# Kernel tuning notes

Measured on AMD Instinct MI355X. Metric: run time of the kernel, lower is better.

Reference implementation:

```python
import jax, jax.numpy as jnp
import numpy as np

N = 4096
Q_DIM = K_DIM = V_DIM = OUT_DIM = ATTN_DIM = 512
NUM_HEADS = 8
HEAD_DIM = ATTN_DIM // NUM_HEADS
SCALE = float(HEAD_DIM) ** (-0.5)


def setup_inputs() -> dict:
    key = jax.random.key(0)
    ks = jax.random.split(key, 12)
    def lin(kw, kb, out_d, in_d):
        bound = 1.0 / np.sqrt(in_d)
        w = jax.random.uniform(kw, (out_d, in_d), jnp.float32, -bound, bound)
        b = jax.random.uniform(kb, (out_d,), jnp.float32, -bound, bound)
        return w, b
    wq_w, wq_b = lin(ks[0], ks[1], ATTN_DIM, Q_DIM)
    wk_w, wk_b = lin(ks[2], ks[3], ATTN_DIM, K_DIM)
    wv_w, wv_b = lin(ks[4], ks[5], ATTN_DIM, V_DIM)
    wo_w, wo_b = lin(ks[6], ks[7], OUT_DIM, ATTN_DIM)
    q = jax.random.normal(ks[8], (N, Q_DIM), jnp.float32)
    k = jax.random.normal(ks[9], (N, K_DIM), jnp.float32)
    v = jax.random.normal(ks[10], (N, V_DIM), jnp.float32)
    mask = jax.random.uniform(ks[11], (N, N)) < 0.1  # True = masked out
    return {"q": q, "k": k, "v": v, "mask": mask,
            "wq_w": wq_w, "wq_b": wq_b, "wk_w": wk_w, "wk_b": wk_b,
            "wv_w": wv_w, "wv_b": wv_b, "wo_w": wo_w, "wo_b": wo_b}


def reference(q, k, v, mask, wq_w, wq_b, wk_w, wk_b, wv_w, wv_b, wo_w, wo_b):
    # Linear projections (torch Linear: x @ W.T + b)
    qp = q @ wq_w.T + wq_b  # (N, A)
    kp = k @ wk_w.T + wk_b
    vp = v @ wv_w.T + wv_b
    # (N, A) -> (H, N, dh)
    qh = qp.reshape(N, NUM_HEADS, HEAD_DIM).transpose(1, 0, 2)
    kh = kp.reshape(N, NUM_HEADS, HEAD_DIM).transpose(1, 0, 2)
    vh = vp.reshape(N, NUM_HEADS, HEAD_DIM).transpose(1, 0, 2)
    attn = jnp.einsum('hnd,hmd->hnm', qh, kh) * SCALE  # (H, N, N)
    attn = jnp.where(mask[None, :, :], jnp.float32(-1e6), attn)
    attn = jax.nn.softmax(attn, axis=-1)
    o = jnp.einsum('hnm,hmd->hnd', attn, vh)  # (H, N, dh)
    o = o.transpose(1, 0, 2).reshape(N, ATTN_DIM)
    return o @ wo_w.T + wo_b  # (N, out_dim)
```

## Files before the change

kernel.cpp:

```cpp
#include <hip/hip_runtime.h>


typedef __attribute__((ext_vector_type(8))) short bf16x8;
typedef __attribute__((ext_vector_type(4))) float f32x4;

#define N_TOK 4096
#define QSCALE 0.18033688f

__device__ __forceinline__ unsigned short f2bf(float f) {
  unsigned u = __float_as_uint(f);
  return (unsigned short)((u + 0x7FFFu + ((u >> 16) & 1u)) >> 16);
}
__device__ __forceinline__ unsigned pack_bf16(float a, float b) {
  unsigned ua = __float_as_uint(a), ub = __float_as_uint(b);
  ua += 0x7FFFu + ((ua >> 16) & 1u);
  ub += 0x7FFFu + ((ub >> 16) & 1u);
  return (ua >> 16) | (ub & 0xFFFF0000u);
}
__device__ __forceinline__ f32x4 mfma16(bf16x8 a, bf16x8 b, f32x4 c) {
  return __builtin_amdgcn_mfma_f32_16x16x32_bf16(a, b, c, 0, 0, 0);
}
__device__ __forceinline__ float fast_exp2(float x) {
#if __has_builtin(__builtin_amdgcn_exp2f)
  return __builtin_amdgcn_exp2f(x);
#else
  return exp2f(x);
#endif
}

__global__ __launch_bounds__(256) void detect_kernel(
    const unsigned* __restrict__ mask, unsigned* __restrict__ flags) {
  __shared__ int s_bad;
  int t = threadIdx.x;
  if (t == 0) s_bad = 0;
  __syncthreads();
  if (mask[t] > 1u) atomicOr(&s_bad, 1);
  __syncthreads();
  if (t == 0) {
    flags[0] = 0;
    flags[1] = s_bad ? 1u : 0u;
  }
}

__global__ __launch_bounds__(256) void pack_mask_kernel(
    const void* __restrict__ m, unsigned long long* __restrict__ bits,
    const unsigned* __restrict__ flags) {
  int gt = blockIdx.x * 256 + threadIdx.x;
  int wave = gt >> 6;
  int lane = threadIdx.x & 63;
  int base = wave * 256;
  unsigned long long b0, b1, b2, b3;
  if (flags[1]) {
    const unsigned char* m8 = (const unsigned char*)m;
    b0 = __ballot(m8[base + 0 * 64 + lane] != 0);
    b1 = __ballot(m8[base + 1 * 64 + lane] != 0);
    b2 = __ballot(m8[base + 2 * 64 + lane] != 0);
    b3 = __ballot(m8[base + 3 * 64 + lane] != 0);
  } else {
    const int* m4 = (const int*)m;
    b0 = __ballot(m4[base + 0 * 64 + lane] != 0);
    b1 = __ballot(m4[base + 1 * 64 + lane] != 0);
    b2 = __ballot(m4[base + 2 * 64 + lane] != 0);
    b3 = __ballot(m4[base + 3 * 64 + lane] != 0);
  }
  if (lane < 4) {
    unsigned long long bl = lane == 0 ? b0 : lane == 1 ? b1 : lane == 2 ? b2 : b3;
    bits[wave * 4 + lane] = bl;
  }
}

template <int F32>
__device__ __forceinline__ void load16(const void* base, int idx,
                                       unsigned short* dst) {
  if (F32) {
    const float* p = (const float*)base + idx;
    float4 f0 = *(const float4*)(p + 0);
    float4 f1 = *(const float4*)(p + 4);
    float4 f2 = *(const float4*)(p + 8);
    float4 f3 = *(const float4*)(p + 12);
    unsigned* d = (unsigned*)dst;
    d[0] = pack_bf16(f0.x, f0.y); d[1] = pack_bf16(f0.z, f0.w);
    d[2] = pack_bf16(f1.x, f1.y); d[3] = pack_bf16(f1.z, f1.w);
    d[4] = pack_bf16(f2.x, f2.y); d[5] = pack_bf16(f2.z, f2.w);
    d[6] = pack_bf16(f3.x, f3.y); d[7] = pack_bf16(f3.z, f3.w);
  } else {
    const unsigned short* p = (const unsigned short*)base + idx;
    *(uint4*)dst = *(const uint4*)p;
    *(uint4*)(dst + 8) = *(const uint4*)(p + 8);
  }
}

template <int A32, int O32, int TRANS>
__device__ __forceinline__ void gemm_body(
    const void* __restrict__ A, const float* __restrict__ W,
    const float* __restrict__ bias, void* __restrict__ out, float oscale) {
  __shared__ unsigned short As[128 * 72];
  __shared__ unsigned short Bs[128 * 72];
  const int t = threadIdx.x;
  const int lane = t & 63, w = t >> 6;
  const int wm = w & 1, wn = w >> 1;
  const int q4 = lane >> 4, i15 = lane & 15;
  const int m0 = blockIdx.y * 128, n0 = blockIdx.x * 128;
  f32x4 acc[4][4] = {};
  const int sr = t >> 2;
  const int sc = (t & 3) * 16;
  for (int k0 = 0; k0 < 512; k0 += 64) {
    __syncthreads();
#pragma unroll
    for (int p = 0; p < 2; ++p) {
      int row = sr + p * 64;
      unsigned short ta[16], tb[16];
      load16<A32>(A, (m0 + row) * 512 + k0 + sc, ta);
      load16<1>(W, (n0 + row) * 512 + k0 + sc, tb);
      *(uint4*)(As + row * 72 + sc) = *(uint4*)ta;
      *(uint4*)(As + row * 72 + sc + 8) = *(uint4*)(ta + 8);
      *(uint4*)(Bs + row * 72 + sc) = *(uint4*)tb;
      *(uint4*)(Bs + row * 72 + sc + 8) = *(uint4*)(tb + 8);
    }
    __syncthreads();
#pragma unroll
    for (int ks = 0; ks < 2; ++ks) {
      bf16x8 af[4], bfr[4];
#pragma unroll
      for (int mt = 0; mt < 4; ++mt)
        af[mt] = *(const bf16x8*)(As + (wm * 64 + mt * 16 + i15) * 72 + q4 * 8 + ks * 32);
#pragma unroll
      for (int nt = 0; nt < 4; ++nt)
        bfr[nt] = *(const bf16x8*)(Bs + (wn * 64 + nt * 16 + i15) * 72 + q4 * 8 + ks * 32);
#pragma unroll
      for (int mt = 0; mt < 4; ++mt)
#pragma unroll
        for (int nt = 0; nt < 4; ++nt)
          acc[mt][nt] = mfma16(af[mt], bfr[nt], acc[mt][nt]);
    }
  }
#pragma unroll
  for (int nt = 0; nt < 4; ++nt) {
    int col = n0 + wn * 64 + nt * 16 + i15;
    float bv = bias[col];
    if (TRANS) {
      unsigned short* ob_ = (unsigned short*)out +
                            (size_t)(col >> 6) * (64 * N_TOK) +
                            (size_t)(col & 63) * N_TOK;
#pragma unroll
      for (int mt = 0; mt < 4; ++mt) {
        int rowb = m0 + wm * 64 + mt * 16 + q4 * 4;
        uint2 pr;
        pr.x = pack_bf16(acc[mt][nt][0] + bv, acc[mt][nt][1] + bv);
        pr.y = pack_bf16(acc[mt][nt][2] + bv, acc[mt][nt][3] + bv);
        *(uint2*)(ob_ + rowb) = pr;
      }
    } else {
#pragma unroll
      for (int mt = 0; mt < 4; ++mt) {
        int rowb = m0 + wm * 64 + mt * 16 + q4 * 4;
#pragma unroll
        for (int rr = 0; rr < 4; ++rr) {
          int idx = (rowb + rr) * 512 + col;
          float val = (acc[mt][nt][rr] + bv) * oscale;
          if (O32) ((float*)out)[idx] = val;
          else ((unsigned short*)out)[idx] = f2bf(val);
        }
      }
    }
  }
}

__global__ __launch_bounds__(256) void qkv_gemm_kernel(
    const float* __restrict__ q, const float* __restrict__ k,
    const float* __restrict__ v, const float* __restrict__ wq,
    const float* __restrict__ wk, const float* __restrict__ wv,
    const float* __restrict__ bq, const float* __restrict__ bk,
    const float* __restrict__ bv, unsigned short* __restrict__ outbase) {
  int z = blockIdx.z;
  if (z == 0) {
    gemm_body<1, 0, 0>(q, wq, bq, outbase, QSCALE);
  } else if (z == 1) {
    gemm_body<1, 0, 0>(k, wk, bk, outbase + (size_t)N_TOK * 512, 1.0f);
  } else {
    gemm_body<1, 0, 1>(v, wv, bv, outbase + 2ull * N_TOK * 512, 1.0f);
  }
}

__global__ __launch_bounds__(256) void out_gemm_kernel(
    const unsigned short* __restrict__ A, const float* __restrict__ W,
    const float* __restrict__ B, float* __restrict__ out) {
  gemm_body<0, 1, 0>(A, W, B, out, 1.0f);
}

__global__ __launch_bounds__(256, 2) void attn_kernel(
    const unsigned short* __restrict__ qp, const unsigned short* __restrict__ kp,
    const unsigned short* __restrict__ vpT,
    const unsigned long long* __restrict__ mbits,
    float* __restrict__ Op, float* __restrict__ dp) {
  __shared__ unsigned short Ks[2][64 * 64];
  __shared__ unsigned short Vt[2][64 * 64];
  const int t = threadIdx.x;
  const int l = t & 63, w = t >> 6;
  const int q4 = l >> 4, i15 = l & 15;
  const int iblk = blockIdx.x * 256;
  const int head = blockIdx.y;
  const int chunk = blockIdx.z;
  const int ch = head * 64;
  const int i0 = iblk + w * 64;
  const int ji = l >> 3;
  const int sg = l & 7;
  const int r0 = w * 2;
  const int j0base = chunk * 1024;
  bf16x8 qf[4][2];
#pragma unroll
  for (int nt = 0; nt < 4; ++nt) {
    const unsigned short* qr = qp + (size_t)(i0 + nt * 16 + i15) * 512 + ch;
#pragma unroll
    for (int ks = 0; ks < 2; ++ks)
      qf[nt][ks] = *(const bf16x8*)(qr + ks * 32 + q4 * 8);
  }
  const unsigned long long* mrow[4];
#pragma unroll
  for (int nt = 0; nt < 4; ++nt)
    mrow[nt] = mbits + (size_t)(i0 + nt * 16 + i15) * 64;
  f32x4 oacc[4][4] = {};
  float den[4] = {0.f, 0.f, 0.f, 0.f};
  const unsigned short* vbase = vpT + (size_t)head * (64 * N_TOK);
  uint4 kst[2], vst[2];
#pragma unroll
  for (int rr = 0; rr < 2; ++rr) {
    int row = (r0 + rr) * 8 + ji;
    kst[rr] = *(const uint4*)(kp + (size_t)(j0base + row) * 512 + ch + sg * 8);
    vst[rr] = *(const uint4*)(vbase + (size_t)row * N_TOK + j0base + sg * 8);
  }
  for (int jt = 0; jt < 16; ++jt) {
    unsigned short* KsB = Ks[jt & 1];
    unsigned short* VtB = Vt[jt & 1];
#pragma unroll
    for (int rr = 0; rr < 2; ++rr) {
      int r = r0 + rr;
      int row = r * 8 + ji;
      *(uint4*)(KsB + row * 64 + ((sg ^ ji ^ r) * 8)) = kst[rr];
      const unsigned* vs = (const unsigned*)&vst[rr];
#pragma unroll
      for (int c2 = 0; c2 < 2; ++c2) {
        int kg = (sg >> 2) * 4 + (sg & 1) * 2 + c2;
        int hh = (sg >> 1) & 1;
        *(uint2*)(VtB + row * 64 + ((kg ^ ji ^ r) * 8) + hh * 4) =
            make_uint2(vs[c2 * 2], vs[c2 * 2 + 1]);
      }
    }
    __syncthreads();
    {
      int jn = j0base + ((jt + 1) & 15) * 64;
#pragma unroll
      for (int rr = 0; rr < 2; ++rr) {
        int row = (r0 + rr) * 8 + ji;
        kst[rr] = *(const uint4*)(kp + (size_t)(jn + row) * 512 + ch + sg * 8);
        vst[rr] = *(const uint4*)(vbase + (size_t)row * N_TOK + jn + sg * 8);
      }
    }
    unsigned long long mw[4];
    int widx = chunk * 16 + jt;
#pragma unroll
    for (int nt = 0; nt < 4; ++nt) mw[nt] = mrow[nt][widx];
    bf16x8 Kf[4][2];
#pragma unroll
    for (int mtj = 0; mtj < 4; ++mtj) {
      int js = mtj * 16 + i15;
#pragma unroll
      for (int ksd = 0; ksd < 2; ++ksd) {
        int g = ksd * 4 + q4;
        Kf[mtj][ksd] =
            *(const bf16x8*)(KsB + js * 64 + ((g ^ (js & 7) ^ (js >> 3)) * 8));
      }
    }
    unsigned pk[4][8];
#pragma unroll
    for (int nt = 0; nt < 4; ++nt) {
      float dsum = 0.f;
#pragma unroll
      for (int mtj = 0; mtj < 4; ++mtj) {
        f32x4 s = {0.f, 0.f, 0.f, 0.f};
        s = mfma16(Kf[mtj][0], qf[nt][0], s);
        s = mfma16(Kf[mtj][1], qf[nt][1], s);
        unsigned nib = (unsigned)(mw[nt] >> (mtj * 16 + q4 * 4)) & 15u;
        float p0 = fast_exp2((nib & 1u) ? -200.f : s[0]);
        float p1 = fast_exp2((nib & 2u) ? -200.f : s[1]);
        float p2 = fast_exp2((nib & 4u) ? -200.f : s[2]);
        float p3 = fast_exp2((nib & 8u) ? -200.f : s[3]);
        dsum += (p0 + p1) + (p2 + p3);
        pk[nt][mtj * 2] = pack_bf16(p0, p1);
        pk[nt][mtj * 2 + 1] = pack_bf16(p2, p3);
      }
      den[nt] += dsum;
    }
    bf16x8 Vf[2][4];
#pragma unroll
    for (int ks = 0; ks < 2; ++ks)
#pragma unroll
      for (int mtd = 0; mtd < 4; ++mtd) {
        int d = mtd * 16 + i15;
        int kg = ks * 4 + q4;
        Vf[ks][mtd] =
            *(const bf16x8*)(VtB + d * 64 + ((kg ^ (d & 7) ^ (d >> 3)) * 8));
      }
#pragma unroll
    for (int nt = 0; nt < 4; ++nt) {
      union { unsigned u[4]; bf16x8 v; } pf0, pf1;
      pf0.u[0] = pk[nt][0]; pf0.u[1] = pk[nt][1];
      pf0.u[2] = pk[nt][2]; pf0.u[3] = pk[nt][3];
      pf1.u[0] = pk[nt][4]; pf1.u[1] = pk[nt][5];
      pf1.u[2] = pk[nt][6]; pf1.u[3] = pk[nt][7];
#pragma unroll
      for (int mtd = 0; mtd < 4; ++mtd) {
        oacc[mtd][nt] = mfma16(Vf[0][mtd], pf0.v, oacc[mtd][nt]);
        oacc[mtd][nt] = mfma16(Vf[1][mtd], pf1.v, oacc[mtd][nt]);
      }
    }
  }
  float* Opc = Op + ((size_t)(chunk * 8 + head) * N_TOK) * 64;
#pragma unroll
  for (int nt = 0; nt < 4; ++nt) {
    float dn = den[nt];
    dn += __shfl_xor(dn, 16);
    dn += __shfl_xor(dn, 32);
    int row = i0 + nt * 16 + i15;
#pragma unroll
    for (int mtd = 0; mtd < 4; ++mtd)
      *(f32x4*)(Opc + (size_t)row * 64 + mtd * 16 + q4 * 4) = oacc[mtd][nt];
    if (q4 == 0) dp[(size_t)(chunk * 8 + head) * N_TOK + row] = dn;
  }
}

__global__ __launch_bounds__(256) void reduce_kernel(
    const float* __restrict__ Op, const float* __restrict__ dp,
    unsigned short* __restrict__ ob) {
  int x = blockIdx.x * 256 + threadIdx.x;
  int i = x >> 7;
  int c = (x & 127) * 4;
  int h = c >> 6;
  int d = c & 63;
  const size_t CH = (size_t)8 * N_TOK * 64;
  size_t base = ((size_t)h * N_TOK + i) * 64 + d;
  float4 a0 = *(const float4*)(Op + base);
  float4 a1 = *(const float4*)(Op + CH + base);
  float4 a2 = *(const float4*)(Op + 2 * CH + base);
  float4 a3 = *(const float4*)(Op + 3 * CH + base);
  float den = dp[(size_t)h * N_TOK + i] + dp[(size_t)(8 + h) * N_TOK + i] +
              dp[(size_t)(16 + h) * N_TOK + i] + dp[(size_t)(24 + h) * N_TOK + i];
  float inv = 1.0f / den;
  float sx = (a0.x + a1.x + a2.x + a3.x) * inv;
  float sy = (a0.y + a1.y + a2.y + a3.y) * inv;
  float sz = (a0.z + a1.z + a2.z + a3.z) * inv;
  float sw = (a0.w + a1.w + a2.w + a3.w) * inv;
  uint2 o;
  o.x = pack_bf16(sx, sy);
  o.y = pack_bf16(sz, sw);
  *(uint2*)(ob + (size_t)i * 512 + c) = o;
}

extern "C" void kernel_launch(void* const* d_in, const int* in_sizes, int n_in,
                              void* d_out, int out_size, void* d_ws, size_t ws_size,
                              hipStream_t stream) {
  const float* q = (const float*)d_in[0];
  const float* k = (const float*)d_in[1];
  const float* v = (const float*)d_in[2];
  const void* mask = d_in[3];
  const float* wq = (const float*)d_in[4];
  const float* bq = (const float*)d_in[5];
  const float* wk = (const float*)d_in[6];
  const float* bk = (const float*)d_in[7];
  const float* wv = (const float*)d_in[8];
  const float* bv = (const float*)d_in[9];
  const float* wo = (const float*)d_in[10];
  const float* bo = (const float*)d_in[11];

  char* ws = (char*)d_ws;
  unsigned* flags = (unsigned*)ws;
  unsigned long long* mb = (unsigned long long*)(ws + 4096);
  unsigned short* qkvp = (unsigned short*)(ws + 4096 + (2ull << 20));
  unsigned short* ob = qkvp + 3ull * N_TOK * 512;
  float* Op = (float*)(ob + (size_t)N_TOK * 512);
  float* dp = Op + 4ull * 8 * N_TOK * 64;

  detect_kernel<<<1, 256, 0, stream>>>((const unsigned*)mask, flags);
  pack_mask_kernel<<<16384, 256, 0, stream>>>(mask, mb, flags);
  qkv_gemm_kernel<<<dim3(4, 32, 3), 256, 0, stream>>>(q, k, v, wq, wk, wv, bq,
                                                      bk, bv, qkvp);
  attn_kernel<<<dim3(16, 8, 4), 256, 0, stream>>>(
      qkvp, qkvp + (size_t)N_TOK * 512, qkvp + 2ull * N_TOK * 512, mb, Op, dp);
  reduce_kernel<<<2048, 256, 0, stream>>>(Op, dp, ob);
  out_gemm_kernel<<<dim3(4, 32), 256, 0, stream>>>(ob, wo, bo, (float*)d_out);
}
```

Before: 264.8 us.

## Pre-convert inputs to bf16, transpose mask bits, prefetch mask words

Adds a separate conversion kernel that turns q/k/v and all weight matrices into bf16 once, so the GEMMs load bf16 directly instead of re-converting fp32 tiles in every block. The packed mask is stored transposed (word-major by row) so attention lanes read coalesced mask words, and the next tile's mask words are prefetched alongside the K/V prefetch. Attention launch bounds are raised to allow three blocks per CU. It adds an extra kernel launch and extra workspace traffic, and the Op buffer now aliases the converted input buffers.

```diff
diff --git a/kernel.cpp b/kernel.cpp
--- a/kernel.cpp
+++ b/kernel.cpp
@@ -43,11 +43,13 @@
 }
 
 __global__ __launch_bounds__(256) void pack_mask_kernel(
-    const void* __restrict__ m, unsigned long long* __restrict__ bits,
+    const void* __restrict__ m, unsigned long long* __restrict__ bitsT,
     const unsigned* __restrict__ flags) {
   int gt = blockIdx.x * 256 + threadIdx.x;
   int wave = gt >> 6;
   int lane = threadIdx.x & 63;
+  int row = wave >> 4;
+  int sub = wave & 15;
   int base = wave * 256;
   unsigned long long b0, b1, b2, b3;
   if (flags[1]) {
@@ -65,34 +67,39 @@
   }
   if (lane < 4) {
     unsigned long long bl = lane == 0 ? b0 : lane == 1 ? b1 : lane == 2 ? b2 : b3;
-    bits[wave * 4 + lane] = bl;
-  }
-}
-
-template <int F32>
-__device__ __forceinline__ void load16(const void* base, int idx,
-                                       unsigned short* dst) {
-  if (F32) {
-    const float* p = (const float*)base + idx;
-    float4 f0 = *(const float4*)(p + 0);
-    float4 f1 = *(const float4*)(p + 4);
-    float4 f2 = *(const float4*)(p + 8);
-    float4 f3 = *(const float4*)(p + 12);
-    unsigned* d = (unsigned*)dst;
-    d[0] = pack_bf16(f0.x, f0.y); d[1] = pack_bf16(f0.z, f0.w);
-    d[2] = pack_bf16(f1.x, f1.y); d[3] = pack_bf16(f1.z, f1.w);
-    d[4] = pack_bf16(f2.x, f2.y); d[5] = pack_bf16(f2.z, f2.w);
-    d[6] = pack_bf16(f3.x, f3.y); d[7] = pack_bf16(f3.z, f3.w);
-  } else {
-    const unsigned short* p = (const unsigned short*)base + idx;
-    *(uint4*)dst = *(const uint4*)p;
-    *(uint4*)(dst + 8) = *(const uint4*)(p + 8);
-  }
-}
-
-template <int A32, int O32, int TRANS>
+    bitsT[(size_t)(sub * 4 + lane) * N_TOK + row] = bl;
+  }
+}
+
+__global__ __launch_bounds__(256) void convert_kernel(
+    const float* __restrict__ s0, const float* __restrict__ s1,
+    const float* __restrict__ s2, const float* __restrict__ s3,
+    const float* __restrict__ s4, const float* __restrict__ s5,
+    const float* __restrict__ s6, unsigned short* __restrict__ d0,
+    unsigned short* __restrict__ d1, unsigned short* __restrict__ d2,
+    unsigned short* __restrict__ d3, unsigned short* __restrict__ d4,
+    unsigned short* __restrict__ d5, unsigned short* __restrict__ d6) {
+  int z = blockIdx.y;
+  int nblk = (z < 3) ? 1024 : 128;
+  if (blockIdx.x >= nblk) return;
+  const float* src = z == 0 ? s0 : z == 1 ? s1 : z == 2 ? s2 : z == 3 ? s3
+                     : z == 4 ? s4 : z == 5 ? s5 : s6;
+  unsigned short* dst = z == 0 ? d0 : z == 1 ? d1 : z == 2 ? d2 : z == 3 ? d3
+                        : z == 4 ? d4 : z == 5 ? d5 : d6;
+  int idx = (blockIdx.x * 256 + threadIdx.x) * 8;
+  float4 f0 = *(const float4*)(src + idx);
+  float4 f1 = *(const float4*)(src + idx + 4);
+  uint4 o;
+  o.x = pack_bf16(f0.x, f0.y);
+  o.y = pack_bf16(f0.z, f0.w);
+  o.z = pack_bf16(f1.x, f1.y);
+  o.w = pack_bf16(f1.z, f1.w);
+  *(uint4*)(dst + idx) = o;
+}
+
+template <int O32, int TRANS>
 __device__ __forceinline__ void gemm_body(
-    const void* __restrict__ A, const float* __restrict__ W,
+    const unsigned short* __restrict__ A, const unsigned short* __restrict__ W,
     const float* __restrict__ bias, void* __restrict__ out, float oscale) {
   __shared__ unsigned short As[128 * 72];
   __shared__ unsigned short Bs[128 * 72];
@@ -109,13 +116,14 @@
 #pragma unroll
     for (int p = 0; p < 2; ++p) {
       int row = sr + p * 64;
-      unsigned short ta[16], tb[16];
-      load16<A32>(A, (m0 + row) * 512 + k0 + sc, ta);
-      load16<1>(W, (n0 + row) * 512 + k0 + sc, tb);
-      *(uint4*)(As + row * 72 + sc) = *(uint4*)ta;
-      *(uint4*)(As + row * 72 + sc + 8) = *(uint4*)(ta + 8);
-      *(uint4*)(Bs + row * 72 + sc) = *(uint4*)tb;
-      *(uint4*)(Bs + row * 72 + sc + 8) = *(uint4*)(tb + 8);
+      const unsigned short* pa = A + (size_t)(m0 + row) * 512 + k0 + sc;
+      const unsigned short* pb = W + (size_t)(n0 + row) * 512 + k0 + sc;
+      uint4 a0 = *(const uint4*)pa, a1 = *(const uint4*)(pa + 8);
+      uint4 b0 = *(const uint4*)pb, b1 = *(const uint4*)(pb + 8);
+      *(uint4*)(As + row * 72 + sc) = a0;
+      *(uint4*)(As + row * 72 + sc + 8) = a1;
+      *(uint4*)(Bs + row * 72 + sc) = b0;
+      *(uint4*)(Bs + row * 72 + sc + 8) = b1;
     }
     __syncthreads();
 #pragma unroll
@@ -167,31 +175,31 @@
 }
 
 __global__ __launch_bounds__(256) void qkv_gemm_kernel(
-    const float* __restrict__ q, const float* __restrict__ k,
-    const float* __restrict__ v, const float* __restrict__ wq,
-    const float* __restrict__ wk, const float* __restrict__ wv,
+    const unsigned short* __restrict__ qc, const unsigned short* __restrict__ kc,
+    const unsigned short* __restrict__ vc, const unsigned short* __restrict__ wqc,
+    const unsigned short* __restrict__ wkc, const unsigned short* __restrict__ wvc,
     const float* __restrict__ bq, const float* __restrict__ bk,
     const float* __restrict__ bv, unsigned short* __restrict__ outbase) {
   int z = blockIdx.z;
   if (z == 0) {
-    gemm_body<1, 0, 0>(q, wq, bq, outbase, QSCALE);
+    gemm_body<0, 0>(qc, wqc, bq, outbase, QSCALE);
   } else if (z == 1) {
-    gemm_body<1, 0, 0>(k, wk, bk, outbase + (size_t)N_TOK * 512, 1.0f);
+    gemm_body<0, 0>(kc, wkc, bk, outbase + (size_t)N_TOK * 512, 1.0f);
   } else {
-    gemm_body<1, 0, 1>(v, wv, bv, outbase + 2ull * N_TOK * 512, 1.0f);
+    gemm_body<0, 1>(vc, wvc, bv, outbase + 2ull * N_TOK * 512, 1.0f);
   }
 }
 
 __global__ __launch_bounds__(256) void out_gemm_kernel(
-    const unsigned short* __restrict__ A, const float* __restrict__ W,
+    const unsigned short* __restrict__ A, const unsigned short* __restrict__ W,
     const float* __restrict__ B, float* __restrict__ out) {
-  gemm_body<0, 1, 0>(A, W, B, out, 1.0f);
-}
-
-__global__ __launch_bounds__(256, 2) void attn_kernel(
+  gemm_body<1, 0>(A, W, B, out, 1.0f);
+}
+
+__global__ __launch_bounds__(256, 3) void attn_kernel(
     const unsigned short* __restrict__ qp, const unsigned short* __restrict__ kp,
     const unsigned short* __restrict__ vpT,
-    const unsigned long long* __restrict__ mbits,
+    const unsigned long long* __restrict__ mbT,
     float* __restrict__ Op, float* __restrict__ dp) {
   __shared__ unsigned short Ks[2][64 * 64];
   __shared__ unsigned short Vt[2][64 * 64];
@@ -215,20 +223,20 @@
     for (int ks = 0; ks < 2; ++ks)
       qf[nt][ks] = *(const bf16x8*)(qr + ks * 32 + q4 * 8);
   }
-  const unsigned long long* mrow[4];
-#pragma unroll
-  for (int nt = 0; nt < 4; ++nt)
-    mrow[nt] = mbits + (size_t)(i0 + nt * 16 + i15) * 64;
   f32x4 oacc[4][4] = {};
   float den[4] = {0.f, 0.f, 0.f, 0.f};
   const unsigned short* vbase = vpT + (size_t)head * (64 * N_TOK);
   uint4 kst[2], vst[2];
+  unsigned long long mwc[4], mwn[4];
 #pragma unroll
   for (int rr = 0; rr < 2; ++rr) {
     int row = (r0 + rr) * 8 + ji;
     kst[rr] = *(const uint4*)(kp + (size_t)(j0base + row) * 512 + ch + sg * 8);
     vst[rr] = *(const uint4*)(vbase + (size_t)row * N_TOK + j0base + sg * 8);
   }
+#pragma unroll
+  for (int nt = 0; nt < 4; ++nt)
+    mwc[nt] = mbT[(size_t)(chunk * 16 + 0) * N_TOK + i0 + nt * 16 + i15];
   for (int jt = 0; jt < 16; ++jt) {
     unsigned short* KsB = Ks[jt & 1];
     unsigned short* VtB = Vt[jt & 1];
@@ -248,18 +256,19 @@
     }
     __syncthreads();
     {
-      int jn = j0base + ((jt + 1) & 15) * 64;
+      int jn = (jt + 1) & 15;
+#pragma unroll
+      for (int nt = 0; nt < 4; ++nt)
+        mwn[nt] =
+            mbT[(size_t)(chunk * 16 + jn) * N_TOK + i0 + nt * 16 + i15];
+      int jng = j0base + jn * 64;
 #pragma unroll
       for (int rr = 0; rr < 2; ++rr) {
         int row = (r0 + rr) * 8 + ji;
-        kst[rr] = *(const uint4*)(kp + (size_t)(jn + row) * 512 + ch + sg * 8);
-        vst[rr] = *(const uint4*)(vbase + (size_t)row * N_TOK + jn + sg * 8);
-      }
-    }
-    unsigned long long mw[4];
-    int widx = chunk * 16 + jt;
-#pragma unroll
-    for (int nt = 0; nt < 4; ++nt) mw[nt] = mrow[nt][widx];
+        kst[rr] = *(const uint4*)(kp + (size_t)(jng + row) * 512 + ch + sg * 8);
+        vst[rr] = *(const uint4*)(vbase + (size_t)row * N_TOK + jng + sg * 8);
+      }
+    }
     bf16x8 Kf[4][2];
 #pragma unroll
     for (int mtj = 0; mtj < 4; ++mtj) {
@@ -280,7 +289,7 @@
         f32x4 s = {0.f, 0.f, 0.f, 0.f};
         s = mfma16(Kf[mtj][0], qf[nt][0], s);
         s = mfma16(Kf[mtj][1], qf[nt][1], s);
-        unsigned nib = (unsigned)(mw[nt] >> (mtj * 16 + q4 * 4)) & 15u;
+        unsigned nib = (unsigned)(mwc[nt] >> (mtj * 16 + q4 * 4)) & 15u;
         float p0 = fast_exp2((nib & 1u) ? -200.f : s[0]);
         float p1 = fast_exp2((nib & 2u) ? -200.f : s[1]);
         float p2 = fast_exp2((nib & 4u) ? -200.f : s[2]);
@@ -314,6 +323,8 @@
         oacc[mtd][nt] = mfma16(Vf[1][mtd], pf1.v, oacc[mtd][nt]);
       }
     }
+#pragma unroll
+    for (int nt = 0; nt < 4; ++nt) mwc[nt] = mwn[nt];
   }
   float* Opc = Op + ((size_t)(chunk * 8 + head) * N_TOK) * 64;
 #pragma unroll
@@ -373,19 +384,29 @@
   const float* bo = (const float*)d_in[11];
 
   char* ws = (char*)d_ws;
+  const size_t MB = 1ull << 20;
   unsigned* flags = (unsigned*)ws;
-  unsigned long long* mb = (unsigned long long*)(ws + 4096);
-  unsigned short* qkvp = (unsigned short*)(ws + 4096 + (2ull << 20));
-  unsigned short* ob = qkvp + 3ull * N_TOK * 512;
-  float* Op = (float*)(ob + (size_t)N_TOK * 512);
-  float* dp = Op + 4ull * 8 * N_TOK * 64;
+  unsigned short* woc = (unsigned short*)(ws + 4096);
+  unsigned long long* mbT = (unsigned long long*)(ws + 1 * MB);
+  unsigned short* qkvp = (unsigned short*)(ws + 3 * MB);
+  unsigned short* ob = (unsigned short*)(ws + 15 * MB);
+  unsigned short* qc = (unsigned short*)(ws + 19 * MB);
+  unsigned short* kc = (unsigned short*)(ws + 23 * MB);
+  unsigned short* vc = (unsigned short*)(ws + 27 * MB);
+  unsigned short* wqc = (unsigned short*)(ws + 31 * MB);
+  unsigned short* wkc = (unsigned short*)(ws + 31 * MB + 512 * 1024);
+  unsigned short* wvc = (unsigned short*)(ws + 32 * MB);
+  float* Op = (float*)(ws + 19 * MB);
+  float* dp = (float*)(ws + 51 * MB);
 
   detect_kernel<<<1, 256, 0, stream>>>((const unsigned*)mask, flags);
-  pack_mask_kernel<<<16384, 256, 0, stream>>>(mask, mb, flags);
-  qkv_gemm_kernel<<<dim3(4, 32, 3), 256, 0, stream>>>(q, k, v, wq, wk, wv, bq,
-                                                      bk, bv, qkvp);
+  pack_mask_kernel<<<16384, 256, 0, stream>>>(mask, mbT, flags);
+  convert_kernel<<<dim3(1024, 7), 256, 0, stream>>>(
+      q, k, v, wq, wk, wv, wo, qc, kc, vc, wqc, wkc, wvc, woc);
+  qkv_gemm_kernel<<<dim3(4, 32, 3), 256, 0, stream>>>(qc, kc, vc, wqc, wkc,
+                                                      wvc, bq, bk, bv, qkvp);
   attn_kernel<<<dim3(16, 8, 4), 256, 0, stream>>>(
-      qkvp, qkvp + (size_t)N_TOK * 512, qkvp + 2ull * N_TOK * 512, mb, Op, dp);
+      qkvp, qkvp + (size_t)N_TOK * 512, qkvp + 2ull * N_TOK * 512, mbT, Op, dp);
   reduce_kernel<<<2048, 256, 0, stream>>>(Op, dp, ob);
-  out_gemm_kernel<<<dim3(4, 32), 256, 0, stream>>>(ob, wo, bo, (float*)d_out);
-}
+  out_gemm_kernel<<<dim3(4, 32), 256, 0, stream>>>(ob, woc, bo, (float*)d_out);
+}
```

Result: slower. 422.7 us (+59.7%).
